# Performance work log

Measured on AMD Instinct MI355X. Metric: run time of the kernel, lower is better.

The kernel has to match this reference:

```python
import math
import jax, jax.numpy as jnp
import numpy as np

B, Q, K, D = 16, 2048, 2048, 128

def setup_inputs() -> dict:
    key = jax.random.key(0)
    kq, kk, kv, kl = jax.random.split(key, 4)
    queries = jax.random.normal(kq, (B, Q, D), dtype=jnp.float32)
    keys = jax.random.normal(kk, (B, K, D), dtype=jnp.float32)
    values = jax.random.normal(kv, (B, K, D), dtype=jnp.float32)
    valid_lens = jax.random.randint(kl, (B,), 0, K, dtype=jnp.int64)
    return {"queries": queries, "keys": keys, "values": values, "valid_lens": valid_lens}

def reference(queries, keys, values, valid_lens):
    d = queries.shape[-1]
    # [B, Q, K] scores
    scores = jnp.einsum("bqd,bkd->bqk", queries, keys) / math.sqrt(d)
    # Original masks X[index][length:] = -1e6, i.e. along the QUERY axis (dim 1),
    # filling entire rows; softmax over the key axis then yields uniform weights
    # for those rows. Reproduce exactly.
    q_idx = jnp.arange(queries.shape[1])  # [Q]
    mask = q_idx[None, :, None] >= valid_lens[:, None, None]  # [B, Q, 1]
    scores = jnp.where(mask, jnp.float32(-1000000.0), scores)
    attention_weights = jax.nn.softmax(scores, axis=-1)
    # dropout p=0.0 (eval) -> identity
    return jnp.einsum("bqk,bkd->bqd", attention_weights, values)
```

## Files before the change

### kernel.cpp

```cpp
#include <hip/hip_runtime.h>
#include <hip/hip_bf16.h>
#include <math.h>


#define Bn 16
#define Qn 2048
#define Kn 2048
#define Dn 128
#define BQ 128
#define SCALE 0.08838834764831845f

typedef _Float16 f16;
typedef _Float16 f16x2_t __attribute__((ext_vector_type(2)));
typedef _Float16 f16x4_t __attribute__((ext_vector_type(4)));
typedef _Float16 f16x8_t __attribute__((ext_vector_type(8)));
typedef float f32x16_t __attribute__((ext_vector_type(16)));

typedef __attribute__((address_space(1))) const unsigned int glb_u32;
typedef __attribute__((address_space(3))) unsigned int lds_u32;

__device__ __forceinline__ void g2l16(const void* g, void* l) {
  __builtin_amdgcn_global_load_lds((glb_u32*)g, (lds_u32*)l, 16, 0, 0);
}


__global__ void __launch_bounds__(256) prep_kernel(
    const float* __restrict__ Kg, const float* __restrict__ Vg,
    f16* __restrict__ Kh, f16* __restrict__ Vt, float* __restrict__ sv) {
  __shared__ float t[32][33];
  __shared__ float ps[8][32];
  const int b = blockIdx.z, k0 = blockIdx.x * 32, d0 = blockIdx.y * 32;
  const int x = threadIdx.x, y = threadIdx.y;

  {
    int lb = (b * 4 + blockIdx.y) * 64 + blockIdx.x;
    size_t off = (size_t)lb * 1024 + (size_t)(y * 32 + x) * 4;
    float4 f = *(const float4*)(Kg + off);
    f16x4_t o;
    o[0] = (f16)f.x; o[1] = (f16)f.y; o[2] = (f16)f.z; o[3] = (f16)f.w;
    size_t k = off >> 7;
    int d4 = (int)(off & 127);
    int G = d4 >> 3;
    int gs = (G & 8) | ((G & 7) ^ ((int)k & 7));
    *(f16x4_t*)(Kh + (k << 7) + (gs << 3) + (d4 & 7)) = o;
  }

  const float* src = Vg + ((size_t)b * Kn + k0) * Dn + d0;
#pragma unroll
  for (int i = 0; i < 4; i++) t[y + 8 * i][x] = src[(size_t)(y + 8 * i) * Dn + x];
  __syncthreads();

#pragma unroll
  for (int i = 0; i < 4; i++) {
    const int k = k0 + x, d = d0 + y + 8 * i;
    const int kb = k >> 7, kk = k & 127;
    const int G = kk >> 3;
    const int gs = (G & 8) | ((G & 7) ^ (d & 7));
    Vt[(((size_t)(b * (Kn / 128) + kb) * 128 + d) << 7) + (gs << 3) + (kk & 7)] =
        (f16)t[x][y + 8 * i];
  }

  float s = 0.f;
#pragma unroll
  for (int i = 0; i < 4; i++) s += t[y + 8 * i][x];
  ps[y][x] = s;
  __syncthreads();
  if (y == 0) {
    float tot = 0.f;
#pragma unroll
    for (int j = 0; j < 8; j++) tot += ps[j][x];
    atomicAdd(&sv[b * Dn + d0 + x], tot);
  }
}

__device__ __forceinline__ int load_vl(const int* __restrict__ vlp, int b) {
  bool is64 = true;
#pragma unroll
  for (int i = 1; i < 16; i += 2) is64 = is64 && (vlp[i] == 0);
  return is64 ? vlp[2 * b] : vlp[b];
}


template <int S>
__global__ void __launch_bounds__(256, 2) flash_kernel(
    const float* __restrict__ Qg, const f16* __restrict__ Kh,
    const f16* __restrict__ Vt, const int* __restrict__ vlp,
    f16* __restrict__ Po, float* __restrict__ Lb) {
  const int b = blockIdx.y;
  const int seg = blockIdx.z;
  const int qt = (blockIdx.x * 5 + seg * 3) & 15;
  const int q0 = qt * BQ;
  const int vl = load_vl(vlp, b);
  if (q0 >= vl) return;

  __shared__ __align__(16) f16 Ks[128 * 128];
  __shared__ __align__(16) f16 Vs[128 * 128];

  const int tid = threadIdx.x;
  const int wave = tid >> 6, lane = tid & 63;
  const int H = lane >> 5, l5 = lane & 31;
  const int qbase = q0 + wave * 32;
  const bool wave_active = qbase < vl;
  const int q_lane = qbase + l5;
  const float sc = (q_lane >= vl) ? 0.f : SCALE;

  const int krow = (l5 & 0x13) | ((l5 & 4) << 1) | ((l5 & 8) >> 1);
  const int krow7 = krow & 7;

  f16x8_t qf[8];
  if (wave_active) {
    const float* qp = Qg + ((size_t)b * Qn + q_lane) * Dn + 8 * H;
#pragma unroll
    for (int s = 0; s < 8; s++) {
      float4 f0 = *(const float4*)(qp + 16 * s);
      float4 f1 = *(const float4*)(qp + 16 * s + 4);
      f16x8_t q8;
      q8[0] = (f16)f0.x; q8[1] = (f16)f0.y; q8[2] = (f16)f0.z; q8[3] = (f16)f0.w;
      q8[4] = (f16)f1.x; q8[5] = (f16)f1.y; q8[6] = (f16)f1.z; q8[7] = (f16)f1.w;
      qf[s] = q8;
    }
  }

  f32x16_t O[4];
#pragma unroll
  for (int i = 0; i < 4; i++) O[i] = (f32x16_t)(0.f);
  float l_lane = 0.f;

  const char* KgT = (const char*)(Kh + (((size_t)b * Kn + (size_t)seg * (Kn / S)) << 7));
  const char* VgT = (const char*)(Vt + (((size_t)(b * (Kn / 128) + seg * (Kn / S) / 128)) << 14));

  for (int it = 0; it < (Kn / S) / 128; it++) {
    __syncthreads();
    const char* kg = KgT + (size_t)it * 32768 + (size_t)(wave * 8) * 1024 + lane * 16;
    const char* vg = VgT + (size_t)it * 32768 + (size_t)(wave * 8) * 1024 + lane * 16;
    f16* kl = Ks + wave * 8 * 512;
    f16* vli = Vs + wave * 8 * 512;
#pragma unroll
    for (int i = 0; i < 8; i++) {
      g2l16(kg + i * 1024, kl + i * 512);
      g2l16(vg + i * 1024, vli + i * 512);
    }
    __syncthreads();

    if (wave_active) {
#pragma unroll
      for (int sub = 0; sub < 4; sub++) {
        f32x16_t Ta = (f32x16_t)(0.f), Tb = (f32x16_t)(0.f);
        const f16* krp = Ks + ((sub * 32 + krow) << 7);
#pragma unroll
        for (int s = 0; s < 8; s += 2) {
          int G0 = 2 * s + H, G1 = 2 * (s + 1) + H;
          int gs0 = (G0 & 8) | ((G0 & 7) ^ krow7);
          int gs1 = (G1 & 8) | ((G1 & 7) ^ krow7);
          f16x8_t kf0 = *(const f16x8_t*)(krp + (gs0 << 3));
          f16x8_t kf1 = *(const f16x8_t*)(krp + (gs1 << 3));
          Ta = __builtin_amdgcn_mfma_f32_32x32x16_f16(kf0, qf[s], Ta, 0, 0, 0);
          Tb = __builtin_amdgcn_mfma_f32_32x32x16_f16(kf1, qf[s + 1], Tb, 0, 0, 0);
        }

        f16x8_t pf0, pf1;
        float ls = 0.f;
#pragma unroll
        for (int r = 0; r < 8; r++) {
          float p = __expf((Ta[r] + Tb[r]) * sc);
          ls += p;
          pf0[r] = (f16)p;
        }
#pragma unroll
        for (int r = 8; r < 16; r++) {
          float p = __expf((Ta[r] + Tb[r]) * sc);
          ls += p;
          pf1[r - 8] = (f16)p;
        }
        l_lane += ls;

#pragma unroll
        for (int dt = 0; dt < 4; dt++) {
          const f16* vrp = Vs + ((dt * 32 + l5) << 7);
          int G0 = sub * 4 + H, G1 = sub * 4 + 2 + H;
          int gs0 = (G0 & 8) | ((G0 & 7) ^ (l5 & 7));
          int gs1 = (G1 & 8) | ((G1 & 7) ^ (l5 & 7));
          f16x8_t vf0 = *(const f16x8_t*)(vrp + (gs0 << 3));
          f16x8_t vf1 = *(const f16x8_t*)(vrp + (gs1 << 3));
          O[dt] = __builtin_amdgcn_mfma_f32_32x32x16_f16(pf0, vf0, O[dt], 0, 0, 0);
          O[dt] = __builtin_amdgcn_mfma_f32_32x32x16_f16(pf1, vf1, O[dt], 0, 0, 0);
        }
      }
    }
  }

  if (!wave_active) return;

  l_lane += __shfl_xor(l_lane, 32);
  if (lane < 32) Lb[(size_t)(seg * Bn + b) * Qn + qbase + l5] = l_lane;

  f16* po = Po + ((size_t)(seg * Bn + b) * Qn + qbase) * Dn;
#pragma unroll
  for (int dt = 0; dt < 4; dt++) {
#pragma unroll
    for (int r = 0; r < 16; r++) {
      const int qrow = (r & 3) + 8 * (r >> 2) + 4 * H;
      po[(size_t)qrow * Dn + dt * 32 + l5] = (f16)O[dt][r];
    }
  }
}


template <int S>
__global__ void __launch_bounds__(256) combine_kernel(
    const f16* __restrict__ Po, const float* __restrict__ Lb,
    const float* __restrict__ sv, const int* __restrict__ vlp,
    float* __restrict__ Out) {
  const int b = blockIdx.y, q0 = blockIdx.x * 64;
  const int vl = load_vl(vlp, b);
  const int tid = threadIdx.x;

  __shared__ float linv[64];
  if (tid < 64) {
    float s = 0.f;
#pragma unroll
    for (int sg = 0; sg < S; sg++) s += Lb[(size_t)(sg * Bn + b) * Qn + q0 + tid];
    linv[tid] = 1.0f / s;
  }
  __syncthreads();

  const int rsub = tid >> 6;
  const int d2 = (tid & 63) * 2;
  const float invK = 1.0f / (float)Kn;
  float2 mv2;
  mv2.x = sv[b * Dn + d2] * invK;
  mv2.y = sv[b * Dn + d2 + 1] * invK;

#pragma unroll
  for (int pass = 0; pass < 16; pass++) {
    const int row = pass * 4 + rsub;
    const int q = q0 + row;
    float2 o;
    if (q >= vl) {
      o = mv2;
    } else {
      float a0 = 0.f, a1 = 0.f;
#pragma unroll
      for (int sg = 0; sg < S; sg++) {
        f16x2_t v = *(const f16x2_t*)(Po + ((size_t)(sg * Bn + b) * Qn + q) * Dn + d2);
        a0 += (float)v[0]; a1 += (float)v[1];
      }
      const float li = linv[row];
      o.x = a0 * li; o.y = a1 * li;
    }
    *(float2*)(Out + ((size_t)b * Qn + q) * Dn + d2) = o;
  }
}


extern "C" void kernel_launch(void* const* d_in, const int* in_sizes, int n_in,
                              void* d_out, int out_size, void* d_ws, size_t ws_size,
                              hipStream_t stream) {
  const float* Qg = (const float*)d_in[0];
  const float* Kg = (const float*)d_in[1];
  const float* Vg = (const float*)d_in[2];
  const int* vl = (const int*)d_in[3];
  float* Out = (float*)d_out;

  char* ws = (char*)d_ws;
  float* sumV = (float*)ws;
  f16* Kh = (f16*)(ws + 8192);
  f16* Vt = (f16*)(ws + 8192 + (size_t)Bn * Kn * Dn * 2);
  const size_t base = 8192 + 2 * (size_t)Bn * Kn * Dn * 2;
  f16* Po = (f16*)(ws + base);

  const size_t po8 = (size_t)8 * Bn * Qn * Dn * 2;
  const size_t lb8 = (size_t)8 * Bn * Qn * 4;
  const size_t po4 = (size_t)4 * Bn * Qn * Dn * 2;
  const size_t need8 = base + po8 + lb8;

  hipMemsetAsync(sumV, 0, Bn * Dn * sizeof(float), stream);
  prep_kernel<<<dim3(64, 4, Bn), dim3(32, 8), 0, stream>>>(Kg, Vg, Kh, Vt, sumV);

  if (ws_size >= need8) {
    float* Lb = (float*)(ws + base + po8);
    flash_kernel<8><<<dim3(16, Bn, 8), 256, 0, stream>>>(Qg, Kh, Vt, vl, Po, Lb);
    combine_kernel<8><<<dim3(Qn / 64, Bn), 256, 0, stream>>>(Po, Lb, sumV, vl, Out);
  } else {
    float* Lb = (float*)(ws + base + po4);
    flash_kernel<4><<<dim3(16, Bn, 4), 256, 0, stream>>>(Qg, Kh, Vt, vl, Po, Lb);
    combine_kernel<4><<<dim3(Qn / 64, Bn), 256, 0, stream>>>(Po, Lb, sumV, vl, Out);
  }
}
```

Measured before the change: 154.8 us.

## Double query tile per wave to reuse K/V fragments; vectorize prep and combine

The flash kernel now gives each wave two 32-row query tiles (256 queries per block), so each K and V fragment read from LDS feeds two MFMAs, halving LDS traffic per FLOP and the number of K/V tile loads across the grid. The QK dot product no longer splits into two partial accumulators over head-dim halves. The prep kernel drops the LDS transpose for V: each thread reads 8 keys down a column and writes one 16-byte f16 vector. K is converted 8 elements per thread. The combine kernel uses 8-wide f16 loads and float4 stores. The doubled register footprint (two Q fragment sets, eight output accumulators) may hurt occupancy under launch_bounds(256,2), and the grid has half as many blocks.

```diff
diff --git a/kernel.cpp b/kernel.cpp
--- a/kernel.cpp
+++ b/kernel.cpp
@@ -7,11 +7,9 @@
 #define Qn 2048
 #define Kn 2048
 #define Dn 128
-#define BQ 128
 #define SCALE 0.08838834764831845f
 
 typedef _Float16 f16;
-typedef _Float16 f16x2_t __attribute__((ext_vector_type(2)));
 typedef _Float16 f16x4_t __attribute__((ext_vector_type(4)));
 typedef _Float16 f16x8_t __attribute__((ext_vector_type(8)));
 typedef float f32x16_t __attribute__((ext_vector_type(16)));
@@ -27,42 +25,43 @@
 __global__ void __launch_bounds__(256) prep_kernel(
     const float* __restrict__ Kg, const float* __restrict__ Vg,
     f16* __restrict__ Kh, f16* __restrict__ Vt, float* __restrict__ sv) {
-  __shared__ float t[32][33];
   __shared__ float ps[8][32];
-  const int b = blockIdx.z, k0 = blockIdx.x * 32, d0 = blockIdx.y * 32;
+  const int b = blockIdx.z;
   const int x = threadIdx.x, y = threadIdx.y;
 
   {
-    int lb = (b * 4 + blockIdx.y) * 64 + blockIdx.x;
-    size_t off = (size_t)lb * 1024 + (size_t)(y * 32 + x) * 4;
-    float4 f = *(const float4*)(Kg + off);
-    f16x4_t o;
-    o[0] = (f16)f.x; o[1] = (f16)f.y; o[2] = (f16)f.z; o[3] = (f16)f.w;
-    size_t k = off >> 7;
-    int d4 = (int)(off & 127);
-    int G = d4 >> 3;
-    int gs = (G & 8) | ((G & 7) ^ ((int)k & 7));
-    *(f16x4_t*)(Kh + (k << 7) + (gs << 3) + (d4 & 7)) = o;
-  }
-
-  const float* src = Vg + ((size_t)b * Kn + k0) * Dn + d0;
-#pragma unroll
-  for (int i = 0; i < 4; i++) t[y + 8 * i][x] = src[(size_t)(y + 8 * i) * Dn + x];
-  __syncthreads();
-
-#pragma unroll
-  for (int i = 0; i < 4; i++) {
-    const int k = k0 + x, d = d0 + y + 8 * i;
-    const int kb = k >> 7, kk = k & 127;
-    const int G = kk >> 3;
+    const int lb = (b * 4 + blockIdx.y) * 32 + blockIdx.x;
+    const int t = y * 32 + x;
+    const size_t key = (size_t)lb * 16 + (t >> 4);
+    const int G = t & 15;
+    const float* kp = Kg + (key << 7) + G * 8;
+    float4 f0 = *(const float4*)kp;
+    float4 f1 = *(const float4*)(kp + 4);
+    f16x8_t o;
+    o[0] = (f16)f0.x; o[1] = (f16)f0.y; o[2] = (f16)f0.z; o[3] = (f16)f0.w;
+    o[4] = (f16)f1.x; o[5] = (f16)f1.y; o[6] = (f16)f1.z; o[7] = (f16)f1.w;
+    const int gs = (G & 8) | ((G & 7) ^ ((int)key & 7));
+    *(f16x8_t*)(Kh + (key << 7) + (gs << 3)) = o;
+  }
+
+  const int k0 = blockIdx.x * 64, d0 = blockIdx.y * 32;
+  const int d = d0 + x;
+  const float* vp = Vg + ((size_t)b * Kn + k0 + y * 8) * Dn + d;
+  float s = 0.f;
+  f16x8_t gr;
+#pragma unroll
+  for (int j = 0; j < 8; j++) {
+    float v = vp[(size_t)j * Dn];
+    s += v;
+    gr[j] = (f16)v;
+  }
+  {
+    const int kb = k0 >> 7;
+    const int G = ((k0 & 64) >> 3) + y;
     const int gs = (G & 8) | ((G & 7) ^ (d & 7));
-    Vt[(((size_t)(b * (Kn / 128) + kb) * 128 + d) << 7) + (gs << 3) + (kk & 7)] =
-        (f16)t[x][y + 8 * i];
-  }
-
-  float s = 0.f;
-#pragma unroll
-  for (int i = 0; i < 4; i++) s += t[y + 8 * i][x];
+    *(f16x8_t*)(Vt + (((size_t)(b * (Kn / 128) + kb) * 128 + d) << 7) + (gs << 3)) = gr;
+  }
+
   ps[y][x] = s;
   __syncthreads();
   if (y == 0) {
@@ -88,8 +87,8 @@
     f16* __restrict__ Po, float* __restrict__ Lb) {
   const int b = blockIdx.y;
   const int seg = blockIdx.z;
-  const int qt = (blockIdx.x * 5 + seg * 3) & 15;
-  const int q0 = qt * BQ;
+  const int qt = (blockIdx.x * 3 + seg * 5) & 7;
+  const int q0 = qt * 256;
   const int vl = load_vl(vlp, b);
   if (q0 >= vl) return;
 
@@ -99,32 +98,41 @@
   const int tid = threadIdx.x;
   const int wave = tid >> 6, lane = tid & 63;
   const int H = lane >> 5, l5 = lane & 31;
-  const int qbase = q0 + wave * 32;
-  const bool wave_active = qbase < vl;
-  const int q_lane = qbase + l5;
-  const float sc = (q_lane >= vl) ? 0.f : SCALE;
+  const int qbA = q0 + wave * 64, qbB = qbA + 32;
+  const bool act = qbA < vl;
+  const int qA = qbA + l5, qB = qbB + l5;
+  const float scA = (qA >= vl) ? 0.f : SCALE;
+  const float scB = (qB >= vl) ? 0.f : SCALE;
 
   const int krow = (l5 & 0x13) | ((l5 & 4) << 1) | ((l5 & 8) >> 1);
   const int krow7 = krow & 7;
 
-  f16x8_t qf[8];
-  if (wave_active) {
-    const float* qp = Qg + ((size_t)b * Qn + q_lane) * Dn + 8 * H;
+  f16x8_t qfA[8], qfB[8];
+  if (act) {
+    const float* qpa = Qg + ((size_t)b * Qn + qA) * Dn + 8 * H;
+    const float* qpb = Qg + ((size_t)b * Qn + qB) * Dn + 8 * H;
 #pragma unroll
     for (int s = 0; s < 8; s++) {
-      float4 f0 = *(const float4*)(qp + 16 * s);
-      float4 f1 = *(const float4*)(qp + 16 * s + 4);
-      f16x8_t q8;
-      q8[0] = (f16)f0.x; q8[1] = (f16)f0.y; q8[2] = (f16)f0.z; q8[3] = (f16)f0.w;
-      q8[4] = (f16)f1.x; q8[5] = (f16)f1.y; q8[6] = (f16)f1.z; q8[7] = (f16)f1.w;
-      qf[s] = q8;
-    }
-  }
-
-  f32x16_t O[4];
-#pragma unroll
-  for (int i = 0; i < 4; i++) O[i] = (f32x16_t)(0.f);
-  float l_lane = 0.f;
+      float4 a0 = *(const float4*)(qpa + 16 * s);
+      float4 a1 = *(const float4*)(qpa + 16 * s + 4);
+      float4 b0 = *(const float4*)(qpb + 16 * s);
+      float4 b1 = *(const float4*)(qpb + 16 * s + 4);
+      f16x8_t fa, fb;
+      fa[0] = (f16)a0.x; fa[1] = (f16)a0.y; fa[2] = (f16)a0.z; fa[3] = (f16)a0.w;
+      fa[4] = (f16)a1.x; fa[5] = (f16)a1.y; fa[6] = (f16)a1.z; fa[7] = (f16)a1.w;
+      fb[0] = (f16)b0.x; fb[1] = (f16)b0.y; fb[2] = (f16)b0.z; fb[3] = (f16)b0.w;
+      fb[4] = (f16)b1.x; fb[5] = (f16)b1.y; fb[6] = (f16)b1.z; fb[7] = (f16)b1.w;
+      qfA[s] = fa; qfB[s] = fb;
+    }
+  }
+
+  f32x16_t OA[4], OB[4];
+#pragma unroll
+  for (int i = 0; i < 4; i++) {
+    OA[i] = (f32x16_t)(0.f);
+    OB[i] = (f32x16_t)(0.f);
+  }
+  float lA = 0.f, lB = 0.f;
 
   const char* KgT = (const char*)(Kh + (((size_t)b * Kn + (size_t)seg * (Kn / S)) << 7));
   const char* VgT = (const char*)(Vt + (((size_t)(b * (Kn / 128) + seg * (Kn / S) / 128)) << 14));
@@ -142,65 +150,73 @@
     }
     __syncthreads();
 
-    if (wave_active) {
+    if (act) {
 #pragma unroll
       for (int sub = 0; sub < 4; sub++) {
-        f32x16_t Ta = (f32x16_t)(0.f), Tb = (f32x16_t)(0.f);
+        f32x16_t TA = (f32x16_t)(0.f), TB = (f32x16_t)(0.f);
         const f16* krp = Ks + ((sub * 32 + krow) << 7);
 #pragma unroll
-        for (int s = 0; s < 8; s += 2) {
-          int G0 = 2 * s + H, G1 = 2 * (s + 1) + H;
-          int gs0 = (G0 & 8) | ((G0 & 7) ^ krow7);
-          int gs1 = (G1 & 8) | ((G1 & 7) ^ krow7);
-          f16x8_t kf0 = *(const f16x8_t*)(krp + (gs0 << 3));
-          f16x8_t kf1 = *(const f16x8_t*)(krp + (gs1 << 3));
-          Ta = __builtin_amdgcn_mfma_f32_32x32x16_f16(kf0, qf[s], Ta, 0, 0, 0);
-          Tb = __builtin_amdgcn_mfma_f32_32x32x16_f16(kf1, qf[s + 1], Tb, 0, 0, 0);
+        for (int s = 0; s < 8; s++) {
+          const int G = 2 * s + H;
+          const int gs = (G & 8) | ((G & 7) ^ krow7);
+          f16x8_t kf = *(const f16x8_t*)(krp + (gs << 3));
+          TA = __builtin_amdgcn_mfma_f32_32x32x16_f16(kf, qfA[s], TA, 0, 0, 0);
+          TB = __builtin_amdgcn_mfma_f32_32x32x16_f16(kf, qfB[s], TB, 0, 0, 0);
         }
 
-        f16x8_t pf0, pf1;
-        float ls = 0.f;
+        f16x8_t pA0, pA1, pB0, pB1;
+        float la = 0.f, lb2 = 0.f;
 #pragma unroll
         for (int r = 0; r < 8; r++) {
-          float p = __expf((Ta[r] + Tb[r]) * sc);
-          ls += p;
-          pf0[r] = (f16)p;
+          float a = __expf(TA[r] * scA);
+          float bq = __expf(TB[r] * scB);
+          la += a; lb2 += bq;
+          pA0[r] = (f16)a; pB0[r] = (f16)bq;
         }
 #pragma unroll
         for (int r = 8; r < 16; r++) {
-          float p = __expf((Ta[r] + Tb[r]) * sc);
-          ls += p;
-          pf1[r - 8] = (f16)p;
+          float a = __expf(TA[r] * scA);
+          float bq = __expf(TB[r] * scB);
+          la += a; lb2 += bq;
+          pA1[r - 8] = (f16)a; pB1[r - 8] = (f16)bq;
         }
-        l_lane += ls;
+        lA += la; lB += lb2;
 
 #pragma unroll
         for (int dt = 0; dt < 4; dt++) {
           const f16* vrp = Vs + ((dt * 32 + l5) << 7);
-          int G0 = sub * 4 + H, G1 = sub * 4 + 2 + H;
-          int gs0 = (G0 & 8) | ((G0 & 7) ^ (l5 & 7));
-          int gs1 = (G1 & 8) | ((G1 & 7) ^ (l5 & 7));
+          const int G0 = sub * 4 + H, G1 = sub * 4 + 2 + H;
+          const int gs0 = (G0 & 8) | ((G0 & 7) ^ (l5 & 7));
+          const int gs1 = (G1 & 8) | ((G1 & 7) ^ (l5 & 7));
           f16x8_t vf0 = *(const f16x8_t*)(vrp + (gs0 << 3));
           f16x8_t vf1 = *(const f16x8_t*)(vrp + (gs1 << 3));
-          O[dt] = __builtin_amdgcn_mfma_f32_32x32x16_f16(pf0, vf0, O[dt], 0, 0, 0);
-          O[dt] = __builtin_amdgcn_mfma_f32_32x32x16_f16(pf1, vf1, O[dt], 0, 0, 0);
+          OA[dt] = __builtin_amdgcn_mfma_f32_32x32x16_f16(pA0, vf0, OA[dt], 0, 0, 0);
+          OA[dt] = __builtin_amdgcn_mfma_f32_32x32x16_f16(pA1, vf1, OA[dt], 0, 0, 0);
+          OB[dt] = __builtin_amdgcn_mfma_f32_32x32x16_f16(pB0, vf0, OB[dt], 0, 0, 0);
+          OB[dt] = __builtin_amdgcn_mfma_f32_32x32x16_f16(pB1, vf1, OB[dt], 0, 0, 0);
         }
       }
     }
   }
 
-  if (!wave_active) return;
-
-  l_lane += __shfl_xor(l_lane, 32);
-  if (lane < 32) Lb[(size_t)(seg * Bn + b) * Qn + qbase + l5] = l_lane;
-
-  f16* po = Po + ((size_t)(seg * Bn + b) * Qn + qbase) * Dn;
+  if (!act) return;
+
+  lA += __shfl_xor(lA, 32);
+  lB += __shfl_xor(lB, 32);
+  if (lane < 32) {
+    Lb[(size_t)(seg * Bn + b) * Qn + qbA + l5] = lA;
+    Lb[(size_t)(seg * Bn + b) * Qn + qbB + l5] = lB;
+  }
+
+  f16* poA = Po + ((size_t)(seg * Bn + b) * Qn + qbA) * Dn;
+  f16* poB = Po + ((size_t)(seg * Bn + b) * Qn + qbB) * Dn;
 #pragma unroll
   for (int dt = 0; dt < 4; dt++) {
 #pragma unroll
     for (int r = 0; r < 16; r++) {
       const int qrow = (r & 3) + 8 * (r >> 2) + 4 * H;
-      po[(size_t)qrow * Dn + dt * 32 + l5] = (f16)O[dt][r];
+      poA[(size_t)qrow * Dn + dt * 32 + l5] = (f16)OA[dt][r];
+      poB[(size_t)qrow * Dn + dt * 32 + l5] = (f16)OB[dt][r];
     }
   }
 }
@@ -224,31 +240,39 @@
   }
   __syncthreads();
 
-  const int rsub = tid >> 6;
-  const int d2 = (tid & 63) * 2;
+  const int row16 = tid >> 4;
+  const int d8 = (tid & 15) * 8;
   const float invK = 1.0f / (float)Kn;
-  float2 mv2;
-  mv2.x = sv[b * Dn + d2] * invK;
-  mv2.y = sv[b * Dn + d2 + 1] * invK;
-
-#pragma unroll
-  for (int pass = 0; pass < 16; pass++) {
-    const int row = pass * 4 + rsub;
+  float mv[8];
+#pragma unroll
+  for (int j = 0; j < 8; j++) mv[j] = sv[b * Dn + d8 + j] * invK;
+
+#pragma unroll
+  for (int pass = 0; pass < 4; pass++) {
+    const int row = pass * 16 + row16;
     const int q = q0 + row;
-    float2 o;
+    float acc[8];
     if (q >= vl) {
-      o = mv2;
+#pragma unroll
+      for (int j = 0; j < 8; j++) acc[j] = mv[j];
     } else {
-      float a0 = 0.f, a1 = 0.f;
+#pragma unroll
+      for (int j = 0; j < 8; j++) acc[j] = 0.f;
 #pragma unroll
       for (int sg = 0; sg < S; sg++) {
-        f16x2_t v = *(const f16x2_t*)(Po + ((size_t)(sg * Bn + b) * Qn + q) * Dn + d2);
-        a0 += (float)v[0]; a1 += (float)v[1];
+        f16x8_t v = *(const f16x8_t*)(Po + ((size_t)(sg * Bn + b) * Qn + q) * Dn + d8);
+#pragma unroll
+        for (int j = 0; j < 8; j++) acc[j] += (float)v[j];
       }
       const float li = linv[row];
-      o.x = a0 * li; o.y = a1 * li;
-    }
-    *(float2*)(Out + ((size_t)b * Qn + q) * Dn + d2) = o;
+#pragma unroll
+      for (int j = 0; j < 8; j++) acc[j] *= li;
+    }
+    float4 o0 = make_float4(acc[0], acc[1], acc[2], acc[3]);
+    float4 o1 = make_float4(acc[4], acc[5], acc[6], acc[7]);
+    float* op = Out + ((size_t)b * Qn + q) * Dn + d8;
+    *(float4*)op = o0;
+    *(float4*)(op + 4) = o1;
   }
 }
 
@@ -275,15 +299,15 @@
   const size_t need8 = base + po8 + lb8;
 
   hipMemsetAsync(sumV, 0, Bn * Dn * sizeof(float), stream);
-  prep_kernel<<<dim3(64, 4, Bn), dim3(32, 8), 0, stream>>>(Kg, Vg, Kh, Vt, sumV);
+  prep_kernel<<<dim3(32, 4, Bn), dim3(32, 8), 0, stream>>>(Kg, Vg, Kh, Vt, sumV);
 
   if (ws_size >= need8) {
     float* Lb = (float*)(ws + base + po8);
-    flash_kernel<8><<<dim3(16, Bn, 8), 256, 0, stream>>>(Qg, Kh, Vt, vl, Po, Lb);
+    flash_kernel<8><<<dim3(8, Bn, 8), 256, 0, stream>>>(Qg, Kh, Vt, vl, Po, Lb);
     combine_kernel<8><<<dim3(Qn / 64, Bn), 256, 0, stream>>>(Po, Lb, sumV, vl, Out);
   } else {
     float* Lb = (float*)(ws + base + po4);
-    flash_kernel<4><<<dim3(16, Bn, 4), 256, 0, stream>>>(Qg, Kh, Vt, vl, Po, Lb);
+    flash_kernel<4><<<dim3(8, Bn, 4), 256, 0, stream>>>(Qg, Kh, Vt, vl, Po, Lb);
     combine_kernel<4><<<dim3(Qn / 64, Bn), 256, 0, stream>>>(Po, Lb, sumV, vl, Out);
   }
 }
```

New measurement: 198.1 us. 28.0% more time.
